# Kernel tuning notes

Measured on AMD Instinct MI355X. Metric: run time of the kernel, lower is better.

Reference implementation:

```python
import jax, jax.numpy as jnp
import numpy as np

N = 50000      # nodes
E = 800000     # edges
D = 128        # input_dim = nb_hidden = emb_dim
A = 4          # nb_edge_types (edge attr dim)
H = 2          # heads (MyGATConv default)
G = 128        # number of graphs (g.batch)
NEG = 0.2      # leaky_relu negative slope
L = 3          # nb_layers


def _glorot(key, shape):
    lim = np.sqrt(6.0 / (shape[-2] + shape[-1]))
    return jax.random.uniform(key, shape, minval=-lim, maxval=lim, dtype=jnp.float32)


def setup_inputs():
    key = jax.random.key(0)
    ks = jax.random.split(key, 20)
    inp = {
        "x": jax.random.normal(ks[0], (N, D), jnp.float32),
        "edge_index": jax.random.randint(ks[1], (2, E), 0, N, dtype=jnp.int32),
        "edge_attr": jax.random.normal(ks[2], (E, A), jnp.float32),
        "batch": jnp.sort(jax.random.randint(ks[3], (N,), 0, G, dtype=jnp.int32)),
    }
    for l in range(L):
        inp[f"linN{l}"] = _glorot(ks[4 + 4 * l], (D, H * D))
        inp[f"linE{l}"] = _glorot(ks[5 + 4 * l], (A, H * A))
        inp[f"att{l}"] = _glorot(ks[6 + 4 * l], (1, H, 2 * D + A))
        inp[f"bias{l}"] = jnp.zeros((H * D,), jnp.float32)
    inp["fw"] = _glorot(ks[16], (D, 1))
    inp["fb"] = jnp.zeros((1,), jnp.float32)
    return inp


def _gat_layer(x_in, e_in, src, dst, linN, linE, att, bias):
    n = x_in.shape[0]
    x = (x_in @ linN + bias).reshape(n, H, D)              # [N,H,D]
    e = (e_in @ linE).reshape(-1, H, A)                    # [E,H,A]
    # alpha = (cat([x_i, x_j, e], -1) * att).sum(-1); x_i = x[src], x_j = x[dst]
    ai = jnp.einsum('nhc,hc->nh', x, att[0, :, :D])        # per-node, gathered at src
    aj = jnp.einsum('nhc,hc->nh', x, att[0, :, D:2 * D])   # per-node, gathered at dst
    ae = jnp.einsum('ehc,hc->eh', e, att[0, :, 2 * D:])
    alpha = jax.nn.leaky_relu(ai[src] + aj[dst] + ae, NEG)  # [E,H]
    # segment softmax over targets (edge_index[1])
    amax = jax.ops.segment_max(alpha, dst, num_segments=n)
    ex = jnp.exp(alpha - amax[dst])
    denom = jax.ops.segment_sum(ex, dst, num_segments=n)
    alpha = ex / denom[dst]
    # PyG propagate: message = alpha * x[src], scatter-add at dst
    msg = alpha[:, :, None] * x[src]                       # [E,H,D]
    out = jax.ops.segment_sum(msg, dst, num_segments=n) + x
    # concat=False -> mean over heads, then ReLU
    return jax.nn.relu(out.mean(axis=1)), jax.nn.relu(e.mean(axis=1))


def reference(x, edge_index, edge_attr, batch,
              linN0, linE0, att0, bias0,
              linN1, linE1, att1, bias1,
              linN2, linE2, att2, bias2,
              fw, fb):
    src, dst = edge_index[0], edge_index[1]
    params = [(linN0, linE0, att0, bias0),
              (linN1, linE1, att1, bias1),
              (linN2, linE2, att2, bias2)]
    h, e = x, edge_attr
    for (lN, lE, at, b) in params:
        h, e = _gat_layer(h, e, src, dst, lN, lE, at, b)
    pooled = jax.ops.segment_sum(h, batch, num_segments=G)  # global_add_pool -> [G,D]
    y = (pooled @ fw + fb).squeeze(-1)                      # [G]
    return y
```

## Files before the change

kernel.cpp:

```cpp
#include <hip/hip_runtime.h>
#include <hip/hip_bf16.h>

#define DD 128
#define AA 4
#define HH 2

typedef short short8 __attribute__((ext_vector_type(8)));
typedef float f32x4 __attribute__((ext_vector_type(4)));

__device__ inline unsigned short f2bf(float f) {
    unsigned u = __float_as_uint(f);
    unsigned r = (u + 0x7fffu + ((u >> 16) & 1u)) >> 16;
    return (unsigned short)r;
}
__device__ inline float4 unpack_bf16x4(uint2 v) {
    float4 r;
    r.x = __uint_as_float(v.x << 16);
    r.y = __uint_as_float(v.x & 0xffff0000u);
    r.z = __uint_as_float(v.y << 16);
    r.w = __uint_as_float(v.y & 0xffff0000u);
    return r;
}
__device__ inline uint2 pack_bf16x4(float a, float b, float c, float d) {
    uint2 p;
    p.x = (unsigned)f2bf(a) | ((unsigned)f2bf(b) << 16);
    p.y = (unsigned)f2bf(c) | ((unsigned)f2bf(d) << 16);
    return p;
}


__global__ void hist_kernel(const int* __restrict__ dst, int* __restrict__ cnt, int E) {
    int e = blockIdx.x * blockDim.x + threadIdx.x;
    if (e < E) atomicAdd(&cnt[dst[e]], 1);
}

__global__ __launch_bounds__(256) void scan1(const int* __restrict__ cnt,
                                             int* __restrict__ bsum, int N) {
    __shared__ int wsh[4];
    int b = blockIdx.x, t = threadIdx.x;
    int lane = t & 63, w = t >> 6;
    int base = b * 1024;
    int v = 0;
    #pragma unroll
    for (int i = 0; i < 4; ++i) {
        int idx = base + i * 256 + t;
        v += (idx < N) ? cnt[idx] : 0;
    }
    #pragma unroll
    for (int o = 32; o; o >>= 1) v += __shfl_xor(v, o);
    if (lane == 0) wsh[w] = v;
    __syncthreads();
    if (t == 0) bsum[b] = wsh[0] + wsh[1] + wsh[2] + wsh[3];
}

__global__ __launch_bounds__(64) void scan2(int* __restrict__ bsum, int NB,
                                            int* __restrict__ total) {
    int t = threadIdx.x;
    int v = (t < NB) ? bsum[t] : 0;
    int x = v;
    #pragma unroll
    for (int o = 1; o < 64; o <<= 1) {
        int u = __shfl_up(x, o);
        if (t >= o) x += u;
    }
    if (t < NB) bsum[t] = x - v;
    if (t == 63) *total = x;
}

__global__ __launch_bounds__(256) void scan3(const int* __restrict__ cnt,
                                             const int* __restrict__ bsum,
                                             int* __restrict__ row_off,
                                             int* __restrict__ cursor, int N) {
    __shared__ int wtot[4];
    __shared__ int carry;
    int b = blockIdx.x, t = threadIdx.x;
    int lane = t & 63, w = t >> 6;
    if (t == 0) carry = bsum[b];
    __syncthreads();
    int base = b * 1024;
    #pragma unroll
    for (int it = 0; it < 4; ++it) {
        int idx = base + it * 256 + t;
        int v = (idx < N) ? cnt[idx] : 0;
        int x = v;
        #pragma unroll
        for (int o = 1; o < 64; o <<= 1) {
            int u = __shfl_up(x, o);
            if (lane >= o) x += u;
        }
        if (lane == 63) wtot[w] = x;
        __syncthreads();
        int woff = 0;
        for (int i = 0; i < w; ++i) woff += wtot[i];
        int c = carry;
        __syncthreads();
        if (t == 255) carry = c + woff + x;
        int ex = c + woff + x - v;
        if (idx < N) { row_off[idx] = ex; cursor[idx] = ex; }
        __syncthreads();
    }
}

__global__ void scatter_kernel(const int* __restrict__ src, const int* __restrict__ dst,
                               int* __restrict__ cursor, int* __restrict__ csr_src,
                               int* __restrict__ pos_of_edge, int E) {
    int e = blockIdx.x * blockDim.x + threadIdx.x;
    if (e >= E) return;
    int p = atomicAdd(&cursor[dst[e]], 1);
    csr_src[p] = src[e];
    pos_of_edge[e] = p;
}


__global__ __launch_bounds__(256) void pack_a0(const float* __restrict__ X,
                                               uint2* __restrict__ As, int N) {
    int t = blockIdx.x * blockDim.x + threadIdx.x;
    if (t >= N * 32) return;
    int r = t >> 5, kq4 = t & 31;
    float4 v = ((const float4*)X)[t];
    int g = r >> 4, m = r & 15;
    int ks = kq4 >> 3, q = (kq4 >> 1) & 3;
    int cell = ((g * 4 + ks) * 4 + q) * 16 + m;
    As[cell * 2 + (kq4 & 1)] = pack_bf16x4(v.x, v.y, v.z, v.w);
}

__global__ __launch_bounds__(256) void pack_w3(const float* __restrict__ W0,
                                               const float* __restrict__ W1,
                                               const float* __restrict__ W2,
                                               unsigned short* __restrict__ Bs) {
    int t = blockIdx.x * blockDim.x + threadIdx.x;
    if (t >= 3 * 128 * 64) return;
    int l = t / (128 * 64);
    int r = t - l * (128 * 64);
    const float* W = (l == 0) ? W0 : (l == 1) ? W1 : W2;
    unsigned short* B = Bs + (size_t)l * 128 * 256;
    int k = r >> 6, c4g = r & 63;
    float4 v = ((const float4*)W)[r];
    int ct = c4g >> 2, n0 = (c4g & 3) * 4;
    int ks = k >> 5, q = (k >> 3) & 3, j = k & 7;
    int cellbase = ((ct * 4 + ks) * 4 + q) * 16 + n0;
    B[(cellbase + 0) * 8 + j] = f2bf(v.x);
    B[(cellbase + 1) * 8 + j] = f2bf(v.y);
    B[(cellbase + 2) * 8 + j] = f2bf(v.z);
    B[(cellbase + 3) * 8 + j] = f2bf(v.w);
}


__global__ __launch_bounds__(256) void gemm_mfma(const short8* __restrict__ As,
                                                 const short8* __restrict__ Bs,
                                                 const float* __restrict__ bias,
                                                 const float* __restrict__ att,
                                                 uint2* __restrict__ xhb,
                                                 float* __restrict__ aiaj, int Ngroups) {
    __shared__ __align__(16) unsigned short sh[4][16 * 260];
    int w = threadIdx.x >> 6;
    int wid = blockIdx.x * 4 + w;
    int lane = threadIdx.x & 63;
    bool active = wid < Ngroups;
    int q = lane >> 4, m = lane & 15;

    if (active) {
        const short8* Ag = As + (size_t)wid * 256;
        f32x4 acc[16];
        #pragma unroll
        for (int ct = 0; ct < 16; ++ct) acc[ct] = (f32x4){0.f, 0.f, 0.f, 0.f};

        #pragma unroll
        for (int ks = 0; ks < 4; ++ks) {
            short8 a = Ag[ks * 64 + lane];
            #pragma unroll
            for (int ct = 0; ct < 16; ++ct) {
                short8 b = Bs[ct * 256 + ks * 64 + lane];
                acc[ct] = __builtin_amdgcn_mfma_f32_16x16x32_bf16(a, b, acc[ct], 0, 0, 0);
            }
        }

        float ai0[4] = {}, ai1[4] = {}, aj0[4] = {}, aj1[4] = {};
        #pragma unroll
        for (int ct = 0; ct < 16; ++ct) {
            int cbase = (ct & 7) * 16 + m;
            const float* atth = att + (ct >= 8 ? (2 * DD + AA) : 0);
            float aS = atth[cbase];
            float aD = atth[DD + cbase];
            float bv = bias[ct * 16 + m];
            #pragma unroll
            for (int reg = 0; reg < 4; ++reg) {
                float val = acc[ct][reg] + bv;
                sh[w][(q * 4 + reg) * 260 + ct * 16 + m] = f2bf(val);
                if (ct < 8) { ai0[reg] += val * aS; aj0[reg] += val * aD; }
                else        { ai1[reg] += val * aS; aj1[reg] += val * aD; }
            }
        }
        #pragma unroll
        for (int o = 1; o < 16; o <<= 1) {
            #pragma unroll
            for (int reg = 0; reg < 4; ++reg) {
                ai0[reg] += __shfl_xor(ai0[reg], o);
                ai1[reg] += __shfl_xor(ai1[reg], o);
                aj0[reg] += __shfl_xor(aj0[reg], o);
                aj1[reg] += __shfl_xor(aj1[reg], o);
            }
        }
        if (m == 0) {
            #pragma unroll
            for (int reg = 0; reg < 4; ++reg) {
                float4 r;
                r.x = ai0[reg]; r.y = ai1[reg]; r.z = aj0[reg]; r.w = aj1[reg];
                ((float4*)aiaj)[wid * 16 + q * 4 + reg] = r;
            }
        }
    }
    __syncthreads();
    if (active) {
        #pragma unroll
        for (int lr = 0; lr < 16; ++lr) {
            uint2 v = *(const uint2*)&sh[w][lr * 260 + lane * 4];
            xhb[(size_t)(wid * 16 + lr) * 64 + lane] = v;
        }
    }
}


__device__ inline void edge_stage(const float4& ev, const float* __restrict__ linE,
                                  const float* __restrict__ att, float2& ae, float4& enext) {
    float eh[8];
    #pragma unroll
    for (int c = 0; c < 8; ++c)
        eh[c] = ev.x * linE[c] + ev.y * linE[8 + c] + ev.z * linE[16 + c] + ev.w * linE[24 + c];
    float a0 = 0.f, a1 = 0.f;
    #pragma unroll
    for (int a = 0; a < 4; ++a) {
        a0 += eh[a]     * att[2 * DD + a];
        a1 += eh[4 + a] * att[(2 * DD + AA) + 2 * DD + a];
    }
    ae.x = a0; ae.y = a1;
    enext.x = fmaxf(0.5f * (eh[0] + eh[4]), 0.f);
    enext.y = fmaxf(0.5f * (eh[1] + eh[5]), 0.f);
    enext.z = fmaxf(0.5f * (eh[2] + eh[6]), 0.f);
    enext.w = fmaxf(0.5f * (eh[3] + eh[7]), 0.f);
}

__global__ __launch_bounds__(256) void edge_all(const float* __restrict__ ein,
                                                const float* __restrict__ linE0, const float* __restrict__ att0,
                                                const float* __restrict__ linE1, const float* __restrict__ att1,
                                                const float* __restrict__ linE2, const float* __restrict__ att2,
                                                const int* __restrict__ pos_of_edge,
                                                float2* __restrict__ ae0,
                                                float2* __restrict__ ae1,
                                                float2* __restrict__ ae2, int E) {
    int e = blockIdx.x * blockDim.x + threadIdx.x;
    if (e >= E) return;
    int p = pos_of_edge[e];
    float4 ev = ((const float4*)ein)[e];
    float2 ae; float4 en;
    edge_stage(ev, linE0, att0, ae, en); ae0[p] = ae;
    edge_stage(en, linE1, att1, ae, ev); ae1[p] = ae;
    edge_stage(ev, linE2, att2, ae, en); ae2[p] = ae;
}


__global__ __launch_bounds__(64) void aggregate(const uint2* __restrict__ xhb,
                                                const float* __restrict__ aiaj,
                                                const float2* __restrict__ ae,
                                                const int* __restrict__ row_off,
                                                const int* __restrict__ csr_src,
                                                uint2* __restrict__ hshuf,
                                                const float* __restrict__ fw,
                                                float* __restrict__ pdots, int N) {
    int d = blockIdx.x;
    int lane = threadIdx.x;
    int s0 = row_off[d], s1 = row_off[d + 1];
    int deg = s1 - s0;
    const float2* aiaj2 = (const float2*)aiaj;
    float2 ajv = aiaj2[d * 2 + 1];

    __shared__ float lex[64][2];
    __shared__ int lsrc[64];
    float4 acc = {0.f, 0.f, 0.f, 0.f};
    float den0 = 0.f, den1 = 0.f;
    int head = lane >> 5;

    for (int c = 0; c < deg; c += 64) {
        int n = min(64, deg - c);
        if (lane < n) {
            int p = s0 + c + lane;
            int s = csr_src[p];
            float2 aiv = aiaj2[s * 2];
            float2 aev = ae[p];
            float a0 = aiv.x + ajv.x + aev.x; a0 = a0 > 0.f ? a0 : 0.2f * a0;
            float a1 = aiv.y + ajv.y + aev.y; a1 = a1 > 0.f ? a1 : 0.2f * a1;
            float e0 = __expf(a0), e1 = __expf(a1);
            den0 += e0; den1 += e1;
            lex[lane][0] = e0; lex[lane][1] = e1;
            lsrc[lane] = s;
        }
        __syncthreads();
        #pragma unroll 4
        for (int j = 0; j < n; ++j) {
            float wgt = lex[j][head];
            float4 xv = unpack_bf16x4(xhb[(size_t)lsrc[j] * 64 + lane]);
            acc.x += wgt * xv.x; acc.y += wgt * xv.y;
            acc.z += wgt * xv.z; acc.w += wgt * xv.w;
        }
        __syncthreads();
    }

    #pragma unroll
    for (int o = 32; o; o >>= 1) {
        den0 += __shfl_xor(den0, o);
        den1 += __shfl_xor(den1, o);
    }
    float den = head ? den1 : den0;
    if (deg == 0) den = 1.0f;
    float inv = 1.0f / den;

    float4 xd = unpack_bf16x4(xhb[(size_t)d * 64 + lane]);
    float4 v;
    v.x = acc.x * inv + xd.x;
    v.y = acc.y * inv + xd.y;
    v.z = acc.z * inv + xd.z;
    v.w = acc.w * inv + xd.w;
    float4 o2;
    o2.x = __shfl_xor(v.x, 32);
    o2.y = __shfl_xor(v.y, 32);
    o2.z = __shfl_xor(v.z, 32);
    o2.w = __shfl_xor(v.w, 32);
    if (lane < 32) {
        float4 r;
        r.x = fmaxf(0.5f * (v.x + o2.x), 0.f);
        r.y = fmaxf(0.5f * (v.y + o2.y), 0.f);
        r.z = fmaxf(0.5f * (v.z + o2.z), 0.f);
        r.w = fmaxf(0.5f * (v.w + o2.w), 0.f);
        if (hshuf) {
            int g = d >> 4, m = d & 15;
            int ks = lane >> 3, q = (lane >> 1) & 3;
            int cell = ((g * 4 + ks) * 4 + q) * 16 + m;
            hshuf[cell * 2 + (lane & 1)] = pack_bf16x4(r.x, r.y, r.z, r.w);
        }
        if (pdots) {
            float4 wv = ((const float4*)fw)[lane];
            float pd = r.x * wv.x + r.y * wv.y + r.z * wv.z + r.w * wv.w;
            #pragma unroll
            for (int o = 16; o; o >>= 1) pd += __shfl_xor(pd, o);
            if (lane == 0) pdots[d] = pd;
        }
    }
}


__global__ __launch_bounds__(256) void segpool_kernel(const float* __restrict__ p,
                                                      const int* __restrict__ batch,
                                                      float* __restrict__ y, int N, int G) {
    __shared__ float bins[128];
    int t = threadIdx.x;
    if (t < G) bins[t] = 0.f;
    __syncthreads();
    int per = (N + gridDim.x - 1) / gridDim.x;
    int lo = blockIdx.x * per;
    int hi = min(lo + per, N);
    float acc = 0.f;
    int key = -1;
    for (int i = lo + t; i < hi; i += 256) {
        int k = batch[i];
        float v = p[i];
        if (k != key) {
            if (key >= 0) atomicAdd(&bins[key], acc);
            key = k;
            acc = 0.f;
        }
        acc += v;
    }
    if (key >= 0) atomicAdd(&bins[key], acc);
    __syncthreads();
    if (t < G && bins[t] != 0.f) atomicAdd(&y[t], bins[t]);
}

__global__ void init_y(float* __restrict__ y, const float* __restrict__ fb, int G) {
    int g = blockIdx.x * blockDim.x + threadIdx.x;
    if (g < G) y[g] = fb[0];
}


extern "C" void kernel_launch(void* const* d_in, const int* in_sizes, int n_in,
                              void* d_out, int out_size, void* d_ws, size_t ws_size,
                              hipStream_t stream) {
    const float* x     = (const float*)d_in[0];
    const int*   ei    = (const int*)d_in[1];
    const float* eattr = (const float*)d_in[2];
    const int*   batch = (const int*)d_in[3];
    const float* fw    = (const float*)d_in[16];
    const float* fb    = (const float*)d_in[17];
    float* y = (float*)d_out;

    const int N = in_sizes[0] / DD;
    const int E = in_sizes[1] / 2;
    const int G = out_size;

    const int* src = ei;
    const int* dst = ei + E;

    char* ws = (char*)d_ws;
    size_t off = 0;
    auto carve = [&](size_t bytes) {
        char* p = ws + off;
        off += (bytes + 255) & ~(size_t)255;
        return p;
    };
    uint2*  xhb     = (uint2*)carve((size_t)N * 256 * 2);
    uint2*  S0      = (uint2*)carve((size_t)N * 128 * 2);
    uint2*  S1      = (uint2*)carve((size_t)N * 128 * 2);
    unsigned short* Bs = (unsigned short*)carve((size_t)3 * 128 * 256 * 2);
    float2* ae0     = (float2*)carve((size_t)E * 2 * 4);
    float2* ae1     = (float2*)carve((size_t)E * 2 * 4);
    float2* ae2     = (float2*)carve((size_t)E * 2 * 4);
    float*  aiaj    = (float*)carve((size_t)N * 4 * 4);
    int*    row_off = (int*)carve((size_t)(N + 1) * 4);
    int*    cursor  = (int*)carve((size_t)N * 4);
    int*    cnt     = (int*)carve((size_t)N * 4);
    int*    csr_src = (int*)carve((size_t)E * 4);
    int*    pos     = (int*)carve((size_t)E * 4);
    float*  pdots   = (float*)carve((size_t)N * 4);
    int*    bsum    = (int*)carve((size_t)256 * 4);

    const int NB = (N + 1023) / 1024;
    const int Ngroups = N / 16;

    hipMemsetAsync(cnt, 0, (size_t)N * 4, stream);
    int eb = (E + 255) / 256;
    hist_kernel<<<eb, 256, 0, stream>>>(dst, cnt, E);
    scan1<<<NB, 256, 0, stream>>>(cnt, bsum, N);
    scan2<<<1, 64, 0, stream>>>(bsum, NB, row_off + N);
    scan3<<<NB, 256, 0, stream>>>(cnt, bsum, row_off, cursor, N);
    scatter_kernel<<<eb, 256, 0, stream>>>(src, dst, cursor, csr_src, pos, E);

    edge_all<<<eb, 256, 0, stream>>>(eattr,
                                     (const float*)d_in[5], (const float*)d_in[6],
                                     (const float*)d_in[9], (const float*)d_in[10],
                                     (const float*)d_in[13], (const float*)d_in[14],
                                     pos, ae0, ae1, ae2, E);

    pack_a0<<<(N * 32 + 255) / 256, 256, 0, stream>>>(x, S0, N);
    pack_w3<<<(3 * 128 * 64 + 255) / 256, 256, 0, stream>>>(
        (const float*)d_in[4], (const float*)d_in[8], (const float*)d_in[12], Bs);

    int gemm_blocks = (Ngroups + 3) / 4;
    float2* aes[3] = {ae0, ae1, ae2};
    uint2* Ain[3]  = {S0, S1, S0};
    uint2* Aout[3] = {S1, S0, nullptr};

    for (int l = 0; l < 3; ++l) {
        const float* att  = (const float*)d_in[6 + 4 * l];
        const float* bias = (const float*)d_in[7 + 4 * l];
        const short8* Bl  = (const short8*)(Bs + (size_t)l * 128 * 256);

        gemm_mfma<<<gemm_blocks, 256, 0, stream>>>((const short8*)Ain[l], Bl,
                                                   bias, att, xhb, aiaj, Ngroups);
        aggregate<<<N, 64, 0, stream>>>(xhb, aiaj, aes[l], row_off, csr_src,
                                        Aout[l], fw, (l == 2) ? pdots : nullptr, N);
    }

    init_y<<<1, 128, 0, stream>>>(y, fb, G);
    segpool_kernel<<<128, 256, 0, stream>>>(pdots, batch, y, N, G);
}
```

Baseline: 521.1 us.

## Fuse CSR build into cooperative kernel and split GEMM per head

Replaces the memset, histogram, three scan kernels, scatter kernel and init_y with one cooperative kernel that uses grid-wide syncs. It also records the original edge id per CSR slot, so edge_all reads edge attributes by gather and writes contiguously. The GEMM now uses two waves per 16-row group, one per head, which halves the accumulator registers and gives more waves. The redundant __syncthreads in the single-wave aggregate kernel are dropped. The cooperative kernel assumes the grid covers N nodes with one thread each and at most 256 scan blocks, so it only holds for inputs up to that size.

```diff
diff --git a/kernel.cpp b/kernel.cpp
--- a/kernel.cpp
+++ b/kernel.cpp
@@ -1,5 +1,8 @@
 #include <hip/hip_runtime.h>
 #include <hip/hip_bf16.h>
+#include <hip/hip_cooperative_groups.h>
+
+namespace cg = cooperative_groups;
 
 #define DD 128
 #define AA 4
@@ -29,86 +32,75 @@
 }
 
 
-__global__ void hist_kernel(const int* __restrict__ dst, int* __restrict__ cnt, int E) {
-    int e = blockIdx.x * blockDim.x + threadIdx.x;
-    if (e < E) atomicAdd(&cnt[dst[e]], 1);
-}
-
-__global__ __launch_bounds__(256) void scan1(const int* __restrict__ cnt,
-                                             int* __restrict__ bsum, int N) {
-    __shared__ int wsh[4];
-    int b = blockIdx.x, t = threadIdx.x;
+__global__ __launch_bounds__(256) void csr_coop(const int* __restrict__ src,
+                                                const int* __restrict__ dst,
+                                                int* __restrict__ cnt,
+                                                int* __restrict__ row_off,
+                                                int* __restrict__ cursor,
+                                                int* __restrict__ csr_src,
+                                                int* __restrict__ csr_eid,
+                                                int* __restrict__ bsum,
+                                                float* __restrict__ y,
+                                                const float* __restrict__ fb,
+                                                int E, int N) {
+    cg::grid_group grid = cg::this_grid();
+    int t = threadIdx.x;
+    int gt = blockIdx.x * 256 + t;
+    const int GT = gridDim.x * 256;
     int lane = t & 63, w = t >> 6;
-    int base = b * 1024;
-    int v = 0;
-    #pragma unroll
-    for (int i = 0; i < 4; ++i) {
-        int idx = base + i * 256 + t;
-        v += (idx < N) ? cnt[idx] : 0;
-    }
-    #pragma unroll
-    for (int o = 32; o; o >>= 1) v += __shfl_xor(v, o);
-    if (lane == 0) wsh[w] = v;
-    __syncthreads();
-    if (t == 0) bsum[b] = wsh[0] + wsh[1] + wsh[2] + wsh[3];
-}
-
-__global__ __launch_bounds__(64) void scan2(int* __restrict__ bsum, int NB,
-                                            int* __restrict__ total) {
-    int t = threadIdx.x;
-    int v = (t < NB) ? bsum[t] : 0;
+    __shared__ int wsum[4];
+    __shared__ int ws2[4];
+
+    for (int i = gt; i < N; i += GT) cnt[i] = 0;
+    if (gt < 128) y[gt] = fb[0];
+    grid.sync();
+
+    for (int e = gt; e < E; e += GT) atomicAdd(&cnt[dst[e]], 1);
+    grid.sync();
+
+    int v = (gt < N) ? cnt[gt] : 0;
     int x = v;
     #pragma unroll
     for (int o = 1; o < 64; o <<= 1) {
         int u = __shfl_up(x, o);
-        if (t >= o) x += u;
-    }
-    if (t < NB) bsum[t] = x - v;
-    if (t == 63) *total = x;
-}
-
-__global__ __launch_bounds__(256) void scan3(const int* __restrict__ cnt,
-                                             const int* __restrict__ bsum,
-                                             int* __restrict__ row_off,
-                                             int* __restrict__ cursor, int N) {
-    __shared__ int wtot[4];
-    __shared__ int carry;
-    int b = blockIdx.x, t = threadIdx.x;
-    int lane = t & 63, w = t >> 6;
-    if (t == 0) carry = bsum[b];
+        if (lane >= o) x += u;
+    }
+    if (lane == 63) wsum[w] = x;
     __syncthreads();
-    int base = b * 1024;
-    #pragma unroll
-    for (int it = 0; it < 4; ++it) {
-        int idx = base + it * 256 + t;
-        int v = (idx < N) ? cnt[idx] : 0;
-        int x = v;
+    int woff = 0;
+    for (int i = 0; i < w; ++i) woff += wsum[i];
+    int incl = x + woff;
+    int btot = wsum[0] + wsum[1] + wsum[2] + wsum[3];
+    if (t == 0) bsum[blockIdx.x] = btot;
+    grid.sync();
+
+    if (blockIdx.x == 0) {
+        int bv = bsum[t];
+        int bx = bv;
         #pragma unroll
         for (int o = 1; o < 64; o <<= 1) {
-            int u = __shfl_up(x, o);
-            if (lane >= o) x += u;
-        }
-        if (lane == 63) wtot[w] = x;
+            int u = __shfl_up(bx, o);
+            if (lane >= o) bx += u;
+        }
+        if (lane == 63) ws2[w] = bx;
         __syncthreads();
-        int woff = 0;
-        for (int i = 0; i < w; ++i) woff += wtot[i];
-        int c = carry;
-        __syncthreads();
-        if (t == 255) carry = c + woff + x;
-        int ex = c + woff + x - v;
-        if (idx < N) { row_off[idx] = ex; cursor[idx] = ex; }
-        __syncthreads();
-    }
-}
-
-__global__ void scatter_kernel(const int* __restrict__ src, const int* __restrict__ dst,
-                               int* __restrict__ cursor, int* __restrict__ csr_src,
-                               int* __restrict__ pos_of_edge, int E) {
-    int e = blockIdx.x * blockDim.x + threadIdx.x;
-    if (e >= E) return;
-    int p = atomicAdd(&cursor[dst[e]], 1);
-    csr_src[p] = src[e];
-    pos_of_edge[e] = p;
+        int wo = 0;
+        for (int i = 0; i < w; ++i) wo += ws2[i];
+        bsum[t] = bx + wo - bv;
+    }
+    grid.sync();
+
+    int base = bsum[blockIdx.x];
+    int ex = base + incl - v;
+    if (gt < N) { row_off[gt] = ex; cursor[gt] = ex; }
+    if (gt == 0) row_off[N] = E;
+    grid.sync();
+
+    for (int e = gt; e < E; e += GT) {
+        int p = atomicAdd(&cursor[dst[e]], 1);
+        csr_src[p] = src[e];
+        csr_eid[p] = e;
+    }
 }
 
 
@@ -152,71 +144,66 @@
                                                  const float* __restrict__ att,
                                                  uint2* __restrict__ xhb,
                                                  float* __restrict__ aiaj, int Ngroups) {
-    __shared__ __align__(16) unsigned short sh[4][16 * 260];
+    __shared__ __align__(16) unsigned short sh[4][16 * 132];
     int w = threadIdx.x >> 6;
-    int wid = blockIdx.x * 4 + w;
+    int flat = blockIdx.x * 4 + w;
+    int wid = flat >> 1, half = flat & 1;
     int lane = threadIdx.x & 63;
-    bool active = wid < Ngroups;
+    if (wid >= Ngroups) return;
     int q = lane >> 4, m = lane & 15;
 
-    if (active) {
-        const short8* Ag = As + (size_t)wid * 256;
-        f32x4 acc[16];
+    const short8* Ag = As + (size_t)wid * 256;
+    f32x4 acc[8];
+    #pragma unroll
+    for (int c8 = 0; c8 < 8; ++c8) acc[c8] = (f32x4){0.f, 0.f, 0.f, 0.f};
+
+    #pragma unroll
+    for (int ks = 0; ks < 4; ++ks) {
+        short8 a = Ag[ks * 64 + lane];
         #pragma unroll
-        for (int ct = 0; ct < 16; ++ct) acc[ct] = (f32x4){0.f, 0.f, 0.f, 0.f};
-
+        for (int c8 = 0; c8 < 8; ++c8) {
+            short8 b = Bs[(half * 8 + c8) * 256 + ks * 64 + lane];
+            acc[c8] = __builtin_amdgcn_mfma_f32_16x16x32_bf16(a, b, acc[c8], 0, 0, 0);
+        }
+    }
+
+    const float* atth = att + half * (2 * DD + AA);
+    float ai[4] = {}, aj[4] = {};
+    #pragma unroll
+    for (int c8 = 0; c8 < 8; ++c8) {
+        int col = c8 * 16 + m;
+        float aS = atth[col];
+        float aD = atth[DD + col];
+        float bv = bias[(half * 8 + c8) * 16 + m];
         #pragma unroll
-        for (int ks = 0; ks < 4; ++ks) {
-            short8 a = Ag[ks * 64 + lane];
-            #pragma unroll
-            for (int ct = 0; ct < 16; ++ct) {
-                short8 b = Bs[ct * 256 + ks * 64 + lane];
-                acc[ct] = __builtin_amdgcn_mfma_f32_16x16x32_bf16(a, b, acc[ct], 0, 0, 0);
-            }
-        }
-
-        float ai0[4] = {}, ai1[4] = {}, aj0[4] = {}, aj1[4] = {};
+        for (int reg = 0; reg < 4; ++reg) {
+            float val = acc[c8][reg] + bv;
+            sh[w][(q * 4 + reg) * 132 + col] = f2bf(val);
+            ai[reg] += val * aS;
+            aj[reg] += val * aD;
+        }
+    }
+    #pragma unroll
+    for (int o = 1; o < 16; o <<= 1) {
         #pragma unroll
-        for (int ct = 0; ct < 16; ++ct) {
-            int cbase = (ct & 7) * 16 + m;
-            const float* atth = att + (ct >= 8 ? (2 * DD + AA) : 0);
-            float aS = atth[cbase];
-            float aD = atth[DD + cbase];
-            float bv = bias[ct * 16 + m];
-            #pragma unroll
-            for (int reg = 0; reg < 4; ++reg) {
-                float val = acc[ct][reg] + bv;
-                sh[w][(q * 4 + reg) * 260 + ct * 16 + m] = f2bf(val);
-                if (ct < 8) { ai0[reg] += val * aS; aj0[reg] += val * aD; }
-                else        { ai1[reg] += val * aS; aj1[reg] += val * aD; }
-            }
-        }
+        for (int reg = 0; reg < 4; ++reg) {
+            ai[reg] += __shfl_xor(ai[reg], o);
+            aj[reg] += __shfl_xor(aj[reg], o);
+        }
+    }
+    if (m == 0) {
         #pragma unroll
-        for (int o = 1; o < 16; o <<= 1) {
-            #pragma unroll
-            for (int reg = 0; reg < 4; ++reg) {
-                ai0[reg] += __shfl_xor(ai0[reg], o);
-                ai1[reg] += __shfl_xor(ai1[reg], o);
-                aj0[reg] += __shfl_xor(aj0[reg], o);
-                aj1[reg] += __shfl_xor(aj1[reg], o);
-            }
-        }
-        if (m == 0) {
-            #pragma unroll
-            for (int reg = 0; reg < 4; ++reg) {
-                float4 r;
-                r.x = ai0[reg]; r.y = ai1[reg]; r.z = aj0[reg]; r.w = aj1[reg];
-                ((float4*)aiaj)[wid * 16 + q * 4 + reg] = r;
-            }
-        }
-    }
-    __syncthreads();
-    if (active) {
-        #pragma unroll
-        for (int lr = 0; lr < 16; ++lr) {
-            uint2 v = *(const uint2*)&sh[w][lr * 260 + lane * 4];
-            xhb[(size_t)(wid * 16 + lr) * 64 + lane] = v;
-        }
+        for (int reg = 0; reg < 4; ++reg) {
+            int row = wid * 16 + q * 4 + reg;
+            aiaj[row * 4 + half] = ai[reg];
+            aiaj[row * 4 + 2 + half] = aj[reg];
+        }
+    }
+    #pragma unroll
+    for (int r2 = 0; r2 < 8; ++r2) {
+        int row = r2 * 2 + (lane >> 5);
+        uint2 v = *(const uint2*)&sh[w][row * 132 + (lane & 31) * 4];
+        xhb[(size_t)(wid * 16 + row) * 64 + half * 32 + (lane & 31)] = v;
     }
 }
 
@@ -244,14 +231,14 @@
                                                 const float* __restrict__ linE0, const float* __restrict__ att0,
                                                 const float* __restrict__ linE1, const float* __restrict__ att1,
                                                 const float* __restrict__ linE2, const float* __restrict__ att2,
-                                                const int* __restrict__ pos_of_edge,
+                                                const int* __restrict__ csr_eid,
                                                 float2* __restrict__ ae0,
                                                 float2* __restrict__ ae1,
                                                 float2* __restrict__ ae2, int E) {
-    int e = blockIdx.x * blockDim.x + threadIdx.x;
-    if (e >= E) return;
-    int p = pos_of_edge[e];
-    float4 ev = ((const float4*)ein)[e];
+    int p = blockIdx.x * blockDim.x + threadIdx.x;
+    if (p >= E) return;
+    int eid = csr_eid[p];
+    float4 ev = ((const float4*)ein)[eid];
     float2 ae; float4 en;
     edge_stage(ev, linE0, att0, ae, en); ae0[p] = ae;
     edge_stage(en, linE1, att1, ae, ev); ae1[p] = ae;
@@ -294,7 +281,6 @@
             lex[lane][0] = e0; lex[lane][1] = e1;
             lsrc[lane] = s;
         }
-        __syncthreads();
         #pragma unroll 4
         for (int j = 0; j < n; ++j) {
             float wgt = lex[j][head];
@@ -302,7 +288,6 @@
             acc.x += wgt * xv.x; acc.y += wgt * xv.y;
             acc.z += wgt * xv.z; acc.w += wgt * xv.w;
         }
-        __syncthreads();
     }
 
     #pragma unroll
@@ -375,11 +360,6 @@
     if (t < G && bins[t] != 0.f) atomicAdd(&y[t], bins[t]);
 }
 
-__global__ void init_y(float* __restrict__ y, const float* __restrict__ fb, int G) {
-    int g = blockIdx.x * blockDim.x + threadIdx.x;
-    if (g < G) y[g] = fb[0];
-}
-
 
 extern "C" void kernel_launch(void* const* d_in, const int* in_sizes, int n_in,
                               void* d_out, int out_size, void* d_ws, size_t ws_size,
@@ -418,32 +398,33 @@
     int*    cursor  = (int*)carve((size_t)N * 4);
     int*    cnt     = (int*)carve((size_t)N * 4);
     int*    csr_src = (int*)carve((size_t)E * 4);
-    int*    pos     = (int*)carve((size_t)E * 4);
+    int*    csr_eid = (int*)carve((size_t)E * 4);
     float*  pdots   = (float*)carve((size_t)N * 4);
     int*    bsum    = (int*)carve((size_t)256 * 4);
 
-    const int NB = (N + 1023) / 1024;
     const int Ngroups = N / 16;
 
-    hipMemsetAsync(cnt, 0, (size_t)N * 4, stream);
+    {
+        int E_ = E, N_ = N;
+        void* args[] = {(void*)&src, (void*)&dst, (void*)&cnt, (void*)&row_off,
+                        (void*)&cursor, (void*)&csr_src, (void*)&csr_eid,
+                        (void*)&bsum, (void*)&y, (void*)&fb, (void*)&E_, (void*)&N_};
+        hipLaunchCooperativeKernel((const void*)csr_coop, dim3(256), dim3(256),
+                                   args, 0, stream);
+    }
+
     int eb = (E + 255) / 256;
-    hist_kernel<<<eb, 256, 0, stream>>>(dst, cnt, E);
-    scan1<<<NB, 256, 0, stream>>>(cnt, bsum, N);
-    scan2<<<1, 64, 0, stream>>>(bsum, NB, row_off + N);
-    scan3<<<NB, 256, 0, stream>>>(cnt, bsum, row_off, cursor, N);
-    scatter_kernel<<<eb, 256, 0, stream>>>(src, dst, cursor, csr_src, pos, E);
-
     edge_all<<<eb, 256, 0, stream>>>(eattr,
                                      (const float*)d_in[5], (const float*)d_in[6],
                                      (const float*)d_in[9], (const float*)d_in[10],
                                      (const float*)d_in[13], (const float*)d_in[14],
-                                     pos, ae0, ae1, ae2, E);
+                                     csr_eid, ae0, ae1, ae2, E);
 
     pack_a0<<<(N * 32 + 255) / 256, 256, 0, stream>>>(x, S0, N);
     pack_w3<<<(3 * 128 * 64 + 255) / 256, 256, 0, stream>>>(
         (const float*)d_in[4], (const float*)d_in[8], (const float*)d_in[12], Bs);
 
-    int gemm_blocks = (Ngroups + 3) / 4;
+    int gemm_blocks = (Ngroups * 2 + 3) / 4;
     float2* aes[3] = {ae0, ae1, ae2};
     uint2* Ain[3]  = {S0, S1, S0};
     uint2* Aout[3] = {S1, S0, nullptr};
@@ -459,6 +440,5 @@
                                         Aout[l], fw, (l == 2) ? pdots : nullptr, N);
     }
 
-    init_y<<<1, 128, 0, stream>>>(y, fb, G);
     segpool_kernel<<<128, 256, 0, stream>>>(pdots, batch, y, N, G);
 }
```

Measured after the change: 654.6 us. 25.6% more time.
